# Kernel optimization log

Measured on AMD Instinct MI355X. Metric: run time of the kernel, lower is better.

## Reference

```python
import jax, jax.numpy as jnp
import numpy as np

TV, B, V = 2048, 16, 1024
TK, K = 2048, 1024


def setup_inputs() -> dict:
    key = jax.random.key(0)
    k1, k2, k3 = jax.random.split(key, 3)
    values = jax.random.normal(k1, (TV, B, V), dtype=jnp.float32)          # time-major values
    values_mask = jnp.ones((B, TV), dtype=jnp.int32)                        # unused by math, kept for fidelity
    keys = jax.random.normal(k2, (B, TK, K), dtype=jnp.float32)
    # xavier-normal-scaled projection weight (created inside torch forward)
    w = jax.random.normal(k3, (K, V), dtype=jnp.float32) * jnp.sqrt(2.0 / (K + V))
    return {"values": values, "values_mask": values_mask, "keys": keys, "w": w}


def reference(values, values_mask, keys, w):
    # values: [Tv, B, V] -> values_t: [B, V, Tv]
    values_t = jnp.transpose(values, (1, 2, 0))
    # project keys: [B, Tk, K] @ [K, V] -> [B, Tk, V] (original loops per batch; vectorized here)
    part_logits = jnp.einsum('btk,kv->btv', keys, w)
    # attn logits: [B, Tk, Tv]
    attn_logits = jnp.einsum('btv,bvs->bts', part_logits, values_t)
    attn_dist = jax.nn.softmax(attn_logits, axis=-1)
    # output: [B, Tk, Tv] @ [B, Tv, V] -> [B, Tk, V]
    output = jnp.einsum('bts,bsv->btv', attn_dist, jnp.transpose(values, (1, 0, 2)))
    return attn_dist, output
```

## Files before the change

kernel.cpp:

```cpp
#include <hip/hip_runtime.h>

#define TV_ 2048
#define NB_ 16
#define NV_ 1024
#define TK_ 2048
#define NK_ 1024

typedef float    f32x4 __attribute__((ext_vector_type(4)));
typedef float    fl4   __attribute__((ext_vector_type(4)));
typedef _Float16 hfx8  __attribute__((ext_vector_type(8)));
typedef ushort   us8   __attribute__((ext_vector_type(8)));

static __device__ __forceinline__ ushort f2h(float f){
  _Float16 h = (_Float16)f;
  return __builtin_bit_cast(ushort, h);
}
static __device__ __forceinline__ float h2f(ushort u){
  return (float)__builtin_bit_cast(_Float16, u);
}

__global__ __launch_bounds__(256) void cvt_h_k(const float* __restrict__ x,
                                               ushort* __restrict__ y, long n4){
  long i = (long)blockIdx.x*256 + threadIdx.x;
  const long stride = (long)gridDim.x*256;
  for (; i < n4; i += stride){
    fl4 v = ((const fl4*)x)[i];
    ((ushort4*)y)[i] = make_ushort4(f2h(v[0]), f2h(v[1]), f2h(v[2]), f2h(v[3]));
  }
}

__global__ void wtrans_k(const float* __restrict__ w, ushort* __restrict__ wT){
  __shared__ float t[32][33];
  const int tx = threadIdx.x, ty = threadIdx.y;
  const int k0 = blockIdx.x*32, v0 = blockIdx.y*32;
#pragma unroll
  for (int r=0;r<4;++r) t[ty+8*r][tx] = w[(long)(k0+ty+8*r)*NV_ + v0+tx];
  __syncthreads();
#pragma unroll
  for (int r=0;r<4;++r)
    wT[(long)(v0+ty+8*r)*NK_ + k0+tx] = f2h(t[tx][ty+8*r]);
}

__global__ void vboth_k(const float* __restrict__ vals,
                        ushort* __restrict__ v2, ushort* __restrict__ vbt){
  __shared__ float t[32][33];
  const int tx = threadIdx.x, ty = threadIdx.y;
  const int s0 = blockIdx.x*32, v0 = blockIdx.y*32, b = blockIdx.z;
#pragma unroll
  for (int r=0;r<4;++r){
    float x = vals[((long)(s0+ty+8*r)*NB_ + b)*NV_ + v0+tx];
    t[ty+8*r][tx] = x;
    v2[((long)b*TV_ + s0+ty+8*r)*NV_ + v0+tx] = f2h(x);
  }
  __syncthreads();
#pragma unroll
  for (int r=0;r<4;++r)
    vbt[((long)b*NV_ + v0+ty+8*r)*TV_ + s0+tx] = f2h(t[tx][ty+8*r]);
}

static __device__ __forceinline__ hfx8 ldfrag(const ushort* base, int r, int q){
  const int off = r*128 + (((q ^ (r & 7)) & 7) << 4);
  return *(const hfx8*)((const char*)base + off);
}

#define SAOFF(b,h) (((b)*2+(h))*8192)
#define SBOFF(b,h) (32768 + ((b)*2+(h))*8192)

#define STAGE(Xp, hb, t, ldsoff) do { \
  _Pragma("unroll") \
  for (int c_=0;c_<2;++c_) \
    __builtin_amdgcn_global_load_lds( \
      (const __attribute__((address_space(1))) unsigned*)((Xp) + (long)(hb)*128*K + (long)(t)*64 + soff[c_]), \
      (__attribute__((address_space(3))) unsigned*)(lds + (ldsoff) + chunk0[c_]*8), 16, 0, 0); \
} while(0)

#define VM4  asm volatile("s_waitcnt vmcnt(4)"  ::: "memory")
#define VM0  asm volatile("s_waitcnt vmcnt(0)"  ::: "memory")
#define NOPS (void)0

#define BARR() do { __builtin_amdgcn_s_barrier(); __builtin_amdgcn_sched_barrier(0); } while(0)

#define MFMA_SET(IB, JB, BREG) \
  _Pragma("unroll") for (int kk=0;kk<2;++kk) \
  _Pragma("unroll") for (int i=0;i<4;++i) \
  _Pragma("unroll") for (int j=0;j<2;++j) \
    acc[(IB)+i][(JB)+j] = __builtin_amdgcn_mfma_f32_16x16x32_f16(aR[i][kk], BREG[j][kk], acc[(IB)+i][(JB)+j], 0,0,0)

#define KTILE(BUF, S0, S1, S2, S3, EW) do { \
  const ushort* sa_ = lds + SAOFF(BUF, wr); \
  const ushort* sb_ = lds + SBOFF(BUF, (wc>>1)); \
  const int brow_ = (wc&1)*64; \
   \
  _Pragma("unroll") for (int i=0;i<4;++i) _Pragma("unroll") for (int kk=0;kk<2;++kk) \
    aR[i][kk] = ldfrag(sa_, i*16+lm, lq+kk*4); \
  _Pragma("unroll") for (int j=0;j<2;++j) _Pragma("unroll") for (int kk=0;kk<2;++kk) \
    b01[j][kk] = ldfrag(sb_, brow_ + j*16 + lm, lq+kk*4); \
  S0; \
  BARR(); \
  __builtin_amdgcn_s_setprio(1); \
  MFMA_SET(0, 0, b01); \
  __builtin_amdgcn_s_setprio(0); \
  BARR(); \
   \
  _Pragma("unroll") for (int j=0;j<2;++j) _Pragma("unroll") for (int kk=0;kk<2;++kk) \
    b23[j][kk] = ldfrag(sb_, brow_ + (2+j)*16 + lm, lq+kk*4); \
  S1; \
  BARR(); \
  __builtin_amdgcn_s_setprio(1); \
  MFMA_SET(0, 2, b23); \
  __builtin_amdgcn_s_setprio(0); \
  BARR(); \
   \
  _Pragma("unroll") for (int i=0;i<4;++i) _Pragma("unroll") for (int kk=0;kk<2;++kk) \
    aR[i][kk] = ldfrag(sa_, (4+i)*16+lm, lq+kk*4); \
  S2; \
  BARR(); \
  __builtin_amdgcn_s_setprio(1); \
  MFMA_SET(4, 2, b23); \
  __builtin_amdgcn_s_setprio(0); \
  BARR(); \
   \
  S3; \
  BARR(); \
  __builtin_amdgcn_s_setprio(1); \
  MFMA_SET(4, 0, b01); \
  __builtin_amdgcn_s_setprio(0); \
  EW; \
  BARR(); \
} while(0)

template<int OUTMODE, int GXL>
__global__ __launch_bounds__(512, 2)
void gemm8_k(const ushort* __restrict__ A, const ushort* __restrict__ BT,
             float* __restrict__ C, ushort* __restrict__ Ch,
             float* __restrict__ pm, float* __restrict__ ps,
             int N, int K, long sA, long sB, long sC)
{
  extern __shared__ ushort lds[];

  const int tid  = threadIdx.x;
  const int lane = tid & 63;
  const int w    = tid >> 6;
  const int wr   = w >> 2;
  const int wc   = w & 3;
  const int lm   = lane & 15, lq = lane >> 4;

  const int bid     = blockIdx.x;
  const int logical = (bid & 7)*((int)gridDim.x >> 3) + (bid >> 3);
  const int bx      = logical & ((1<<GXL)-1);
  const int by      = (logical >> GXL) & 7;
  const int bz      = logical >> (GXL+3);
  const long m0     = (long)by * 256;
  const long n0     = (long)bx * 256;

  const ushort* Ap = A  + (long)bz*sA + m0*K;
  const ushort* Bp = BT + (long)bz*sB + n0*K;

  int chunk0[2], soff[2];
#pragma unroll
  for (int c=0;c<2;++c){
    chunk0[c] = (w<<7) + (c<<6);
    const int idx = chunk0[c] + lane;
    const int row = idx >> 3, sl = idx & 7;
    soff[c] = row*K + ((sl ^ (row & 7)) << 3);
  }

  f32x4 acc[8][4];
#pragma unroll
  for (int i=0;i<8;++i)
#pragma unroll
    for (int j=0;j<4;++j) acc[i][j] = (f32x4){0.f,0.f,0.f,0.f};

  hfx8 aR[4][2], b01[2][2], b23[2][2];

  const int NT = K >> 6;

  STAGE(Ap, 0, 0, SAOFF(0,0));
  STAGE(Ap, 1, 0, SAOFF(0,1));
  STAGE(Bp, 0, 0, SBOFF(0,0));
  STAGE(Bp, 1, 0, SBOFF(0,1));
  STAGE(Bp, 0, 1, SBOFF(1,0));
  STAGE(Ap, 0, 1, SAOFF(1,0));
  VM4;
  BARR();

  for (int u=0; u <= NT-4; u+=2){
    KTILE(0,
          STAGE(Ap, 1, u+1, SAOFF(1,1)),
          STAGE(Bp, 1, u+1, SBOFF(1,1)),
          STAGE(Bp, 0, u+2, SBOFF(0,0)),
          STAGE(Ap, 0, u+2, SAOFF(0,0)),
          VM4);
    KTILE(1,
          STAGE(Ap, 1, u+2, SAOFF(0,1)),
          STAGE(Bp, 1, u+2, SBOFF(0,1)),
          STAGE(Bp, 0, u+3, SBOFF(1,0)),
          STAGE(Ap, 0, u+3, SAOFF(1,0)),
          VM4);
  }
  KTILE(0,
        STAGE(Ap, 1, NT-1, SAOFF(1,1)),
        STAGE(Bp, 1, NT-1, SBOFF(1,1)),
        NOPS, NOPS, VM0);
  KTILE(1, NOPS, NOPS, NOPS, NOPS, NOPS);

  const long cb = (long)bz*sC;
  if constexpr (OUTMODE == 2){
#pragma unroll
    for (int i=0;i<8;++i){
      float mts[4];
#pragma unroll
      for (int g=0; g<4; ++g){
        float mt = fmaxf(fmaxf(acc[i][0][g], acc[i][1][g]), fmaxf(acc[i][2][g], acc[i][3][g]));
#pragma unroll
        for (int off=1; off<16; off<<=1) mt = fmaxf(mt, __shfl_xor(mt, off));
        float se = 0.f;
#pragma unroll
        for (int j=0;j<4;++j) se += __expf(acc[i][j][g] - mt);
#pragma unroll
        for (int off=1; off<16; off<<=1) se += __shfl_xor(se, off);
        if (lm == 0){
          const long rg = (long)bz*TK_ + m0 + wr*128 + i*16 + lq*4 + g;
          pm[rg*32 + bx*4 + wc] = mt;
          ps[rg*32 + bx*4 + wc] = se;
        }
        mts[g] = mt;
      }
#pragma unroll
      for (int j=0;j<4;++j)
#pragma unroll
        for (int g=0; g<4; ++g){
          const long gm = m0 + wr*128 + i*16 + lq*4 + g;
          const long gn = n0 + wc*64  + j*16 + lm;
          Ch[cb + gm*N + gn] = f2h(acc[i][j][g] - mts[g]);
        }
    }
  } else {
#pragma unroll
    for (int i=0;i<8;++i)
#pragma unroll
      for (int j=0;j<4;++j)
#pragma unroll
        for (int g=0; g<4; ++g){
          const long gm = m0 + wr*128 + i*16 + lq*4 + g;
          const long gn = n0 + wc*64  + j*16 + lm;
          const long o = cb + gm*N + gn;
          if constexpr (OUTMODE == 1) Ch[o] = f2h(acc[i][j][g]);
          else                        C[o]  = acc[i][j][g];
        }
  }
}

__global__ __launch_bounds__(256) void rs_k(const float* __restrict__ pm,
                                            const float* __restrict__ ps,
                                            float* __restrict__ dsh2){
  const long r = (long)blockIdx.x*256 + threadIdx.x;
  float pmv[32];
  float m = -3.4e38f;
#pragma unroll
  for (int p=0;p<32;++p){ pmv[p] = pm[r*32+p]; m = fmaxf(m, pmv[p]); }
  float s = 0.f;
#pragma unroll
  for (int p=0;p<32;++p) s += ps[r*32+p] * __expf(pmv[p] - m);
  const float lg = __logf(s);
#pragma unroll
  for (int p=0;p<32;++p) dsh2[r*32+p] = pmv[p] - m - lg;
}

__global__ __launch_bounds__(256) void pexp_k(const ushort* __restrict__ h16,
                                              const float* __restrict__ dsh2,
                                              float* __restrict__ attn,
                                              ushort* __restrict__ p16){
  const long n8 = (long)NB_*TK_*TV_/8;
  long i = (long)blockIdx.x*256 + threadIdx.x;
  const long stride = (long)gridDim.x*256;
  for (; i < n8; i += stride){
    us8 hv = ((const us8*)h16)[i];
    const long row = i >> 8;
    const int  c8  = (int)(i & 255);
    const float d = dsh2[row*32 + (c8>>3)];
    float p[8];
#pragma unroll
    for (int e=0;e<8;++e) p[e] = __expf(h2f((ushort)hv[e]) + d);
    fl4 q0 = {p[0],p[1],p[2],p[3]}, q1 = {p[4],p[5],p[6],p[7]};
    *(fl4*)(attn + i*8)     = q0;
    *(fl4*)(attn + i*8 + 4) = q1;
    us8 o;
#pragma unroll
    for (int e=0;e<8;++e) o[e] = f2h(p[e]);
    ((us8*)p16)[i] = o;
  }
}

__global__ __launch_bounds__(256) void softmax_k(float* __restrict__ lg, ushort* __restrict__ pb){
  const long base = (long)blockIdx.x * TV_;
  const int tid = threadIdx.x;
  const int lane = tid & 63, w = tid >> 6;
  float x[8];
  fl4 a = *(const fl4*)(lg + base + tid*8);
  fl4 b = *(const fl4*)(lg + base + tid*8 + 4);
  x[0]=a[0];x[1]=a[1];x[2]=a[2];x[3]=a[3];x[4]=b[0];x[5]=b[1];x[6]=b[2];x[7]=b[3];
  float m = x[0];
#pragma unroll
  for (int j=1;j<8;++j) m = fmaxf(m, x[j]);
#pragma unroll
  for (int off=32; off; off>>=1) m = fmaxf(m, __shfl_xor(m, off));
  __shared__ float rm[4], rs[4];
  if (lane==0) rm[w]=m;
  __syncthreads();
  m = fmaxf(fmaxf(rm[0],rm[1]), fmaxf(rm[2],rm[3]));
  float s = 0.f;
#pragma unroll
  for (int j=0;j<8;++j){ x[j] = __expf(x[j]-m); s += x[j]; }
#pragma unroll
  for (int off=32; off; off>>=1) s += __shfl_xor(s, off);
  if (lane==0) rs[w]=s;
  __syncthreads();
  s = rs[0]+rs[1]+rs[2]+rs[3];
  const float inv = 1.f/s;
  fl4 p0 = {x[0]*inv, x[1]*inv, x[2]*inv, x[3]*inv};
  fl4 p1 = {x[4]*inv, x[5]*inv, x[6]*inv, x[7]*inv};
  *(fl4*)(lg + base + tid*8)     = p0;
  *(fl4*)(lg + base + tid*8 + 4) = p1;
  *(ushort4*)(pb + base + tid*8)     = make_ushort4(f2h(p0[0]),f2h(p0[1]),f2h(p0[2]),f2h(p0[3]));
  *(ushort4*)(pb + base + tid*8 + 4) = make_ushort4(f2h(p1[0]),f2h(p1[1]),f2h(p1[2]),f2h(p1[3]));
}

extern "C" void kernel_launch(void* const* d_in, const int* in_sizes, int n_in,
                              void* d_out, int out_size, void* d_ws, size_t ws_size,
                              hipStream_t stream){
  (void)in_sizes; (void)n_in; (void)out_size;
  const float* values = (const float*)d_in[0];
  const float* keys   = (const float*)d_in[2];
  const float* w      = (const float*)d_in[3];

  float* attn = (float*)d_out;
  float* outp = (float*)d_out + (long)NB_*TK_*TV_;

  char* ws = (char*)d_ws;
  const long MB = 1024L*1024L;
  const bool fused = ws_size >= (size_t)(340*MB);
  const size_t LDSB = 131072;

  if (fused){
    ushort* kh   = (ushort*)(ws);
    ushort* vbt  = (ushort*)(ws + 64*MB);
    ushort* plh  = (ushort*)(ws + 128*MB);
    ushort* adb  = (ushort*)(ws + 192*MB);
    float*  pm   = (float*)(ws + 320*MB);
    float*  psum = (float*)(ws + 324*MB);
    float*  dsh2 = (float*)(ws + 328*MB);
    ushort* wth  = (ushort*)(ws + 332*MB);
    ushort* v2   = kh;
    ushort* p16  = plh;
    p16 = adb;

    cvt_h_k<<<2048,256,0,stream>>>(keys, kh, (long)NB_*TK_*NK_/4);
    wtrans_k<<<dim3(32,32),dim3(32,8),0,stream>>>(w, wth);
    gemm8_k<1,2><<<512,512,LDSB,stream>>>(
        kh, wth, nullptr, plh, nullptr, nullptr,
        NV_, NK_, (long)TK_*NK_, 0L, (long)TK_*NV_);
    vboth_k<<<dim3(TV_/32, NV_/32, NB_),dim3(32,8),0,stream>>>(values, v2, vbt);
    gemm8_k<2,3><<<1024,512,LDSB,stream>>>(
        plh, v2, nullptr, adb, pm, psum,
        TV_, NV_, (long)TK_*NV_, (long)TV_*NV_, (long)TK_*TV_);
    rs_k<<<NB_*TK_/256,256,0,stream>>>(pm, psum, dsh2);
    pexp_k<<<2048,256,0,stream>>>(adb, dsh2, attn, p16);
    gemm8_k<0,2><<<512,512,LDSB,stream>>>(
        p16, vbt, outp, nullptr, nullptr, nullptr,
        NV_, TV_, (long)TK_*TV_, (long)NV_*TV_, (long)TK_*NV_);
  } else {
    ushort* kh  = (ushort*)(ws);
    ushort* vbt = (ushort*)(ws + 64*MB);
    ushort* plh = (ushort*)(ws + 128*MB);
    ushort* adb = (ushort*)(ws + 128*MB);
    ushort* wth = (ushort*)(ws + 256*MB);
    ushort* v2  = kh;

    cvt_h_k<<<2048,256,0,stream>>>(keys, kh, (long)NB_*TK_*NK_/4);
    wtrans_k<<<dim3(32,32),dim3(32,8),0,stream>>>(w, wth);
    gemm8_k<1,2><<<512,512,LDSB,stream>>>(
        kh, wth, nullptr, plh, nullptr, nullptr,
        NV_, NK_, (long)TK_*NK_, 0L, (long)TK_*NV_);
    vboth_k<<<dim3(TV_/32, NV_/32, NB_),dim3(32,8),0,stream>>>(values, v2, vbt);
    gemm8_k<0,3><<<1024,512,LDSB,stream>>>(
        plh, v2, attn, nullptr, nullptr, nullptr,
        TV_, NV_, (long)TK_*NV_, (long)TV_*NV_, (long)TK_*TV_);
    softmax_k<<<NB_*TK_,256,0,stream>>>(attn, adb);
    gemm8_k<0,2><<<512,512,LDSB,stream>>>(
        adb, vbt, outp, nullptr, nullptr, nullptr,
        NV_, TV_, (long)TK_*TV_, (long)NV_*TV_, (long)TK_*NV_);
  }
}
```

Before: 608.5 us.

## Switch GEMM core to 32x32x16 MFMA with new LDS swizzle and 3D grid

Replaces the 16x16x32 MFMA tiling with 32x32x16 f16 MFMAs. Each wave now holds 4x2 32x32 accumulators and loads fewer, larger fragments per k-step. The LDS XOR swizzle gains an extra row-dependent term so the new fragment reads avoid bank conflicts. The XCD-aware block remapping is dropped in favour of a plain 3D grid, and the softmax-partials epilogue is rewritten for the 32-row output layout. Giving up the XCD remap may hurt L2 locality across chiplets.

```diff
diff --git a/kernel.cpp b/kernel.cpp
--- a/kernel.cpp
+++ b/kernel.cpp
@@ -6,10 +6,11 @@
 #define TK_ 2048
 #define NK_ 1024
 
-typedef float    f32x4 __attribute__((ext_vector_type(4)));
-typedef float    fl4   __attribute__((ext_vector_type(4)));
-typedef _Float16 hfx8  __attribute__((ext_vector_type(8)));
-typedef ushort   us8   __attribute__((ext_vector_type(8)));
+typedef float    f32x4  __attribute__((ext_vector_type(4)));
+typedef float    f32x16 __attribute__((ext_vector_type(16)));
+typedef float    fl4    __attribute__((ext_vector_type(4)));
+typedef _Float16 hfx8   __attribute__((ext_vector_type(8)));
+typedef ushort   us8    __attribute__((ext_vector_type(8)));
 
 static __device__ __forceinline__ ushort f2h(float f){
   _Float16 h = (_Float16)f;
@@ -58,9 +59,9 @@
     vbt[((long)b*NV_ + v0+ty+8*r)*TV_ + s0+tx] = f2h(t[tx][ty+8*r]);
 }
 
-static __device__ __forceinline__ hfx8 ldfrag(const ushort* base, int r, int q){
-  const int off = r*128 + (((q ^ (r & 7)) & 7) << 4);
-  return *(const hfx8*)((const char*)base + off);
+static __device__ __forceinline__ hfx8 ldfrag32(const ushort* base, int r, int g){
+  const int slot = (g ^ (r & 7) ^ ((r >> 2) & 6)) & 7;
+  return *(const hfx8*)((const char*)base + r*128 + (slot << 4));
 }
 
 #define SAOFF(b,h) (((b)*2+(h))*8192)
@@ -80,56 +81,55 @@
 
 #define BARR() do { __builtin_amdgcn_s_barrier(); __builtin_amdgcn_sched_barrier(0); } while(0)
 
-#define MFMA_SET(IB, JB, BREG) \
-  _Pragma("unroll") for (int kk=0;kk<2;++kk) \
-  _Pragma("unroll") for (int i=0;i<4;++i) \
-  _Pragma("unroll") for (int j=0;j<2;++j) \
-    acc[(IB)+i][(JB)+j] = __builtin_amdgcn_mfma_f32_16x16x32_f16(aR[i][kk], BREG[j][kk], acc[(IB)+i][(JB)+j], 0,0,0)
+#define MFMA32(I0, JB, BREG) \
+  _Pragma("unroll") for (int s_=0;s_<4;++s_) \
+  _Pragma("unroll") for (int i_=0;i_<2;++i_) \
+    acc32[(I0)+i_][JB] = __builtin_amdgcn_mfma_f32_32x32x16_f16(aF[i_][s_], BREG[s_], acc32[(I0)+i_][JB], 0,0,0)
 
 #define KTILE(BUF, S0, S1, S2, S3, EW) do { \
   const ushort* sa_ = lds + SAOFF(BUF, wr); \
   const ushort* sb_ = lds + SBOFF(BUF, (wc>>1)); \
   const int brow_ = (wc&1)*64; \
    \
-  _Pragma("unroll") for (int i=0;i<4;++i) _Pragma("unroll") for (int kk=0;kk<2;++kk) \
-    aR[i][kk] = ldfrag(sa_, i*16+lm, lq+kk*4); \
-  _Pragma("unroll") for (int j=0;j<2;++j) _Pragma("unroll") for (int kk=0;kk<2;++kk) \
-    b01[j][kk] = ldfrag(sb_, brow_ + j*16 + lm, lq+kk*4); \
+  _Pragma("unroll") for (int i_=0;i_<2;++i_) _Pragma("unroll") for (int s_=0;s_<4;++s_) \
+    aF[i_][s_] = ldfrag32(sa_, i_*32 + l31, s_*2 + lhi); \
+  _Pragma("unroll") for (int s_=0;s_<4;++s_) \
+    bj0[s_] = ldfrag32(sb_, brow_ + l31, s_*2 + lhi); \
   S0; \
   BARR(); \
   __builtin_amdgcn_s_setprio(1); \
-  MFMA_SET(0, 0, b01); \
+  MFMA32(0, 0, bj0); \
   __builtin_amdgcn_s_setprio(0); \
   BARR(); \
    \
-  _Pragma("unroll") for (int j=0;j<2;++j) _Pragma("unroll") for (int kk=0;kk<2;++kk) \
-    b23[j][kk] = ldfrag(sb_, brow_ + (2+j)*16 + lm, lq+kk*4); \
+  _Pragma("unroll") for (int s_=0;s_<4;++s_) \
+    bj1[s_] = ldfrag32(sb_, brow_ + 32 + l31, s_*2 + lhi); \
   S1; \
   BARR(); \
   __builtin_amdgcn_s_setprio(1); \
-  MFMA_SET(0, 2, b23); \
+  MFMA32(0, 1, bj1); \
   __builtin_amdgcn_s_setprio(0); \
   BARR(); \
    \
-  _Pragma("unroll") for (int i=0;i<4;++i) _Pragma("unroll") for (int kk=0;kk<2;++kk) \
-    aR[i][kk] = ldfrag(sa_, (4+i)*16+lm, lq+kk*4); \
+  _Pragma("unroll") for (int i_=0;i_<2;++i_) _Pragma("unroll") for (int s_=0;s_<4;++s_) \
+    aF[i_][s_] = ldfrag32(sa_, (2+i_)*32 + l31, s_*2 + lhi); \
   S2; \
   BARR(); \
   __builtin_amdgcn_s_setprio(1); \
-  MFMA_SET(4, 2, b23); \
+  MFMA32(2, 1, bj1); \
   __builtin_amdgcn_s_setprio(0); \
   BARR(); \
    \
   S3; \
   BARR(); \
   __builtin_amdgcn_s_setprio(1); \
-  MFMA_SET(4, 0, b01); \
+  MFMA32(2, 0, bj0); \
   __builtin_amdgcn_s_setprio(0); \
   EW; \
   BARR(); \
 } while(0)
 
-template<int OUTMODE, int GXL>
+template<int OUTMODE>
 __global__ __launch_bounds__(512, 2)
 void gemm8_k(const ushort* __restrict__ A, const ushort* __restrict__ BT,
              float* __restrict__ C, ushort* __restrict__ Ch,
@@ -143,15 +143,10 @@
   const int w    = tid >> 6;
   const int wr   = w >> 2;
   const int wc   = w & 3;
-  const int lm   = lane & 15, lq = lane >> 4;
-
-  const int bid     = blockIdx.x;
-  const int logical = (bid & 7)*((int)gridDim.x >> 3) + (bid >> 3);
-  const int bx      = logical & ((1<<GXL)-1);
-  const int by      = (logical >> GXL) & 7;
-  const int bz      = logical >> (GXL+3);
-  const long m0     = (long)by * 256;
-  const long n0     = (long)bx * 256;
+  const int l31  = lane & 31, lhi = lane >> 5;
+  const int bz   = blockIdx.z;
+  const long m0  = (long)blockIdx.y * 256;
+  const long n0  = (long)blockIdx.x * 256;
 
   const ushort* Ap = A  + (long)bz*sA + m0*K;
   const ushort* Bp = BT + (long)bz*sB + n0*K;
@@ -162,16 +157,18 @@
     chunk0[c] = (w<<7) + (c<<6);
     const int idx = chunk0[c] + lane;
     const int row = idx >> 3, sl = idx & 7;
-    soff[c] = row*K + ((sl ^ (row & 7)) << 3);
-  }
-
-  f32x4 acc[8][4];
-#pragma unroll
-  for (int i=0;i<8;++i)
-#pragma unroll
-    for (int j=0;j<4;++j) acc[i][j] = (f32x4){0.f,0.f,0.f,0.f};
-
-  hfx8 aR[4][2], b01[2][2], b23[2][2];
+    soff[c] = row*K + (((sl ^ (row & 7) ^ ((row >> 2) & 6)) & 7) << 3);
+  }
+
+  f32x16 acc32[4][2];
+#pragma unroll
+  for (int i=0;i<4;++i)
+#pragma unroll
+    for (int j=0;j<2;++j)
+#pragma unroll
+      for (int r=0;r<16;++r) acc32[i][j][r] = 0.f;
+
+  hfx8 aF[2][4], bj0[4], bj1[4];
 
   const int NT = K >> 6;
 
@@ -207,46 +204,47 @@
   const long cb = (long)bz*sC;
   if constexpr (OUTMODE == 2){
 #pragma unroll
-    for (int i=0;i<8;++i){
-      float mts[4];
-#pragma unroll
-      for (int g=0; g<4; ++g){
-        float mt = fmaxf(fmaxf(acc[i][0][g], acc[i][1][g]), fmaxf(acc[i][2][g], acc[i][3][g]));
-#pragma unroll
-        for (int off=1; off<16; off<<=1) mt = fmaxf(mt, __shfl_xor(mt, off));
-        float se = 0.f;
-#pragma unroll
-        for (int j=0;j<4;++j) se += __expf(acc[i][j][g] - mt);
-#pragma unroll
-        for (int off=1; off<16; off<<=1) se += __shfl_xor(se, off);
-        if (lm == 0){
-          const long rg = (long)bz*TK_ + m0 + wr*128 + i*16 + lq*4 + g;
-          pm[rg*32 + bx*4 + wc] = mt;
-          ps[rg*32 + bx*4 + wc] = se;
+    for (int i=0;i<4;++i){
+      float mts[16];
+#pragma unroll
+      for (int r=0;r<16;++r){
+        float mt = fmaxf(acc32[i][0][r], acc32[i][1][r]);
+#pragma unroll
+        for (int off=1; off<32; off<<=1) mt = fmaxf(mt, __shfl_xor(mt, off));
+        float se = __expf(acc32[i][0][r] - mt) + __expf(acc32[i][1][r] - mt);
+#pragma unroll
+        for (int off=1; off<32; off<<=1) se += __shfl_xor(se, off);
+        if (l31 == 0){
+          const int row = (r&3) + 8*(r>>2) + 4*lhi;
+          const long rg = (long)bz*TK_ + m0 + wr*128 + i*32 + row;
+          pm[rg*32 + blockIdx.x*4 + wc] = mt;
+          ps[rg*32 + blockIdx.x*4 + wc] = se;
         }
-        mts[g] = mt;
+        mts[r] = mt;
       }
 #pragma unroll
-      for (int j=0;j<4;++j)
-#pragma unroll
-        for (int g=0; g<4; ++g){
-          const long gm = m0 + wr*128 + i*16 + lq*4 + g;
-          const long gn = n0 + wc*64  + j*16 + lm;
-          Ch[cb + gm*N + gn] = f2h(acc[i][j][g] - mts[g]);
+      for (int j=0;j<2;++j)
+#pragma unroll
+        for (int r=0;r<16;++r){
+          const int row = (r&3) + 8*(r>>2) + 4*lhi;
+          const long gm = m0 + wr*128 + i*32 + row;
+          const long gn = n0 + wc*64  + j*32 + l31;
+          Ch[cb + gm*N + gn] = f2h(acc32[i][j][r] - mts[r]);
         }
     }
   } else {
 #pragma unroll
-    for (int i=0;i<8;++i)
-#pragma unroll
-      for (int j=0;j<4;++j)
-#pragma unroll
-        for (int g=0; g<4; ++g){
-          const long gm = m0 + wr*128 + i*16 + lq*4 + g;
-          const long gn = n0 + wc*64  + j*16 + lm;
+    for (int i=0;i<4;++i)
+#pragma unroll
+      for (int j=0;j<2;++j)
+#pragma unroll
+        for (int r=0;r<16;++r){
+          const int row = (r&3) + 8*(r>>2) + 4*lhi;
+          const long gm = m0 + wr*128 + i*32 + row;
+          const long gn = n0 + wc*64  + j*32 + l31;
           const long o = cb + gm*N + gn;
-          if constexpr (OUTMODE == 1) Ch[o] = f2h(acc[i][j][g]);
-          else                        C[o]  = acc[i][j][g];
+          if constexpr (OUTMODE == 1) Ch[o] = f2h(acc32[i][j][r]);
+          else                        C[o]  = acc32[i][j][r];
         }
   }
 }
@@ -352,21 +350,20 @@
     float*  dsh2 = (float*)(ws + 328*MB);
     ushort* wth  = (ushort*)(ws + 332*MB);
     ushort* v2   = kh;
-    ushort* p16  = plh;
-    p16 = adb;
+    ushort* p16  = adb;
 
     cvt_h_k<<<2048,256,0,stream>>>(keys, kh, (long)NB_*TK_*NK_/4);
     wtrans_k<<<dim3(32,32),dim3(32,8),0,stream>>>(w, wth);
-    gemm8_k<1,2><<<512,512,LDSB,stream>>>(
+    gemm8_k<1><<<dim3(NV_/256, TK_/256, NB_),512,LDSB,stream>>>(
         kh, wth, nullptr, plh, nullptr, nullptr,
         NV_, NK_, (long)TK_*NK_, 0L, (long)TK_*NV_);
     vboth_k<<<dim3(TV_/32, NV_/32, NB_),dim3(32,8),0,stream>>>(values, v2, vbt);
-    gemm8_k<2,3><<<1024,512,LDSB,stream>>>(
+    gemm8_k<2><<<dim3(TV_/256, TK_/256, NB_),512,LDSB,stream>>>(
         plh, v2, nullptr, adb, pm, psum,
         TV_, NV_, (long)TK_*NV_, (long)TV_*NV_, (long)TK_*TV_);
     rs_k<<<NB_*TK_/256,256,0,stream>>>(pm, psum, dsh2);
     pexp_k<<<2048,256,0,stream>>>(adb, dsh2, attn, p16);
-    gemm8_k<0,2><<<512,512,LDSB,stream>>>(
+    gemm8_k<0><<<dim3(NV_/256, TK_/256, NB_),512,LDSB,stream>>>(
         p16, vbt, outp, nullptr, nullptr, nullptr,
         NV_, TV_, (long)TK_*TV_, (long)NV_*TV_, (long)TK_*NV_);
   } else {
@@ -379,15 +376,15 @@
 
     cvt_h_k<<<2048,256,0,stream>>>(keys, kh, (long)NB_*TK_*NK_/4);
     wtrans_k<<<dim3(32,32),dim3(32,8),0,stream>>>(w, wth);
-    gemm8_k<1,2><<<512,512,LDSB,stream>>>(
+    gemm8_k<1><<<dim3(NV_/256, TK_/256, NB_),512,LDSB,stream>>>(
         kh, wth, nullptr, plh, nullptr, nullptr,
         NV_, NK_, (long)TK_*NK_, 0L, (long)TK_*NV_);
     vboth_k<<<dim3(TV_/32, NV_/32, NB_),dim3(32,8),0,stream>>>(values, v2, vbt);
-    gemm8_k<0,3><<<1024,512,LDSB,stream>>>(
+    gemm8_k<0><<<dim3(TV_/256, TK_/256, NB_),512,LDSB,stream>>>(
         plh, v2, attn, nullptr, nullptr, nullptr,
         TV_, NV_, (long)TK_*NV_, (long)TV_*NV_, (long)TK_*TV_);
     softmax_k<<<NB_*TK_,256,0,stream>>>(attn, adb);
-    gemm8_k<0,2><<<512,512,LDSB,stream>>>(
+    gemm8_k<0><<<dim3(NV_/256, TK_/256, NB_),512,LDSB,stream>>>(
         adb, vbt, outp, nullptr, nullptr, nullptr,
         NV_, TV_, (long)TK_*TV_, (long)NV_*TV_, (long)TK_*NV_);
   }
```

Result: slower. 702.0 us (+15.4%).
